# Kernel tuning notes

Hardware: AMD Instinct MI355X
Metric: run time of the kernel (lower is better)

Reference implementation:

```python
import jax, jax.numpy as jnp
import numpy as np

B, S, H, KV, D = 1, 2048, 32, 8, 128
HID = H * D
SINK, WIN, POOL = 128, 1024, 100
TAU = 1.0


def setup_inputs() -> dict:
    key = jax.random.key(0)
    ks = jax.random.split(key, 12)
    init = lambda k, shape: jax.random.normal(k, shape, jnp.float32) * 0.02
    return dict(
        hidden_states=jax.random.normal(ks[0], (B, S, HID), jnp.float32),
        Wq=init(ks[1], (HID, HID)),
        Wk=init(ks[2], (HID, KV * D)),
        Wv=init(ks[3], (HID, KV * D)),
        Wo=init(ks[4], (HID, HID)),
        fe1_w=init(ks[5], (D, 8 * D)), fe1_b=jnp.zeros((8 * D,), jnp.float32),
        fe2_w=init(ks[6], (8 * D, 2 * D)), fe2_b=jnp.zeros((2 * D,), jnp.float32),
        r1_w=init(ks[7], (2 * D, 4 * D)), r1_b=jnp.zeros((4 * D,), jnp.float32),
        r2_w=init(ks[8], (4 * D, D)), r2_b=jnp.zeros((D,), jnp.float32),
        r3_w=init(ks[9], (D, 1)), r3_b=jnp.zeros((1,), jnp.float32),
        router_noise=jax.random.uniform(ks[10], (B, 1), jnp.float32),
    )


def _rope(x):
    # x: [B,S,h,D]; non-interleaved (rotate-half) RoPE, base 10000
    half = D // 2
    inv_freq = 1.0 / (10000.0 ** (jnp.arange(0, D, 2, dtype=jnp.float32) / D))
    t = jnp.arange(S, dtype=jnp.float32)
    freqs = jnp.outer(t, inv_freq)  # [S, half]
    cos = jnp.cos(freqs)[None, :, None, :]
    sin = jnp.sin(freqs)[None, :, None, :]
    x1, x2 = x[..., :half], x[..., half:]
    return jnp.concatenate([x1 * cos - x2 * sin, x2 * cos + x1 * sin], axis=-1)


def reference(hidden_states, Wq, Wk, Wv, Wo, fe1_w, fe1_b, fe2_w, fe2_b,
              r1_w, r1_b, r2_w, r2_b, r3_w, r3_b, router_noise):
    q = (hidden_states @ Wq).reshape(B, S, H, D)
    k = (hidden_states @ Wk).reshape(B, S, KV, D)
    v = (hidden_states @ Wv).reshape(B, S, KV, D)
    q = _rope(q)
    k = _rope(k)
    # GQA: repeat kv heads
    kr = jnp.repeat(k, H // KV, axis=2)
    vr = jnp.repeat(v, H // KV, axis=2)
    scale = 1.0 / jnp.sqrt(jnp.float32(D))
    scores = jnp.einsum('bshd,bthd->bhst', q, kr) * scale  # [B,H,S,S]
    i = jnp.arange(S)[:, None]
    j = jnp.arange(S)[None, :]
    causal = j <= i
    # sink tokens + sliding window (streaming-LLM pattern)
    stream = causal & ((j < SINK) | (j > i - WIN))
    neg = jnp.float32(-1e30)
    p_full = jax.nn.softmax(jnp.where(causal, scores, neg), axis=-1)
    p_strm = jax.nn.softmax(jnp.where(stream, scores, neg), axis=-1)
    o_full = jnp.einsum('bhst,bthd->bshd', p_full, vr)
    o_strm = jnp.einsum('bhst,bthd->bshd', p_strm, vr)
    # Router: ctx_q pooling over first/last POOL query positions -> [B,H,D] -> [B,D]
    pooled = jnp.concatenate([q[:, :POOL], q[:, -POOL:]], axis=1).mean(axis=1)
    feat = pooled.mean(axis=1)  # [B,D]
    h1 = jax.nn.silu(feat @ fe1_w + fe1_b)
    h2 = h1 @ fe2_w + fe2_b
    h3 = jax.nn.silu(h2 @ r1_w + r1_b)
    h4 = jax.nn.silu(h3 @ r2_w + r2_b)
    logits = h4 @ r3_w + r3_b  # [B,1]
    eps = 1e-8
    g = -jnp.log(-jnp.log(router_noise + eps) + eps)
    z_soft = jax.nn.sigmoid((logits + g) / TAU)
    z_hard = (z_soft > 0.5).astype(z_soft.dtype)
    z = z_hard + z_soft - jax.lax.stop_gradient(z_soft)  # straight-through
    mix = z.reshape(B, 1, 1, 1)
    o = mix * o_strm + (1.0 - mix) * o_full  # gate sparse vs full retrieval
    return o.reshape(B, S, HID) @ Wo
```

## Files before the change

kernel.cpp:

```cpp
#include <hip/hip_runtime.h>
#include <hip/hip_bf16.h>

typedef unsigned short u16;
typedef unsigned int u32;
typedef __bf16 bf16x8 __attribute__((ext_vector_type(8)));
typedef float f32x4 __attribute__((ext_vector_type(4)));
typedef unsigned short u16x8 __attribute__((ext_vector_type(8)));

#define S_ 2048
#define H_ 32
#define KV_ 8
#define D_ 128
#define HID_ 4096
#define KVD_ 1024
#define QKVN 6144
#define SINK_ 128
#define WIN_ 1024
#define POOL_ 100
#define KVB 64

__device__ __forceinline__ u16 f2bf(float f) {
  union { float f; u32 u; } v; v.f = f;
  u32 r = v.u + 0x7FFFu + ((v.u >> 16) & 1u);
  return (u16)(r >> 16);
}
__device__ __forceinline__ float bf2f(u16 h) {
  union { u32 u; float f; } v; v.u = ((u32)h) << 16;
  return v.f;
}
__device__ __forceinline__ void glds16(const void* g, void* l) {
  __builtin_amdgcn_global_load_lds((__attribute__((address_space(1))) void*)g,
                                   (__attribute__((address_space(3))) void*)l, 16, 0, 0);
}

__device__ __forceinline__ void tr64(const float* __restrict__ W, u16* __restrict__ Wt,
                                     int K, int N, int nt, int kt, int tid, u16 T[64][66]) {
  const int r = tid >> 4, c4 = tid & 15;
#pragma unroll
  for (int p = 0; p < 4; ++p) {
    int row = p * 16 + r;
    float4 v = *(const float4*)&W[(size_t)(kt * 64 + row) * N + nt * 64 + c4 * 4];
    T[row][c4 * 4 + 0] = f2bf(v.x);
    T[row][c4 * 4 + 1] = f2bf(v.y);
    T[row][c4 * 4 + 2] = f2bf(v.z);
    T[row][c4 * 4 + 3] = f2bf(v.w);
  }
  __syncthreads();
  const int n = tid >> 3, c8 = tid & 7;
#pragma unroll
  for (int p = 0; p < 2; ++p) {
    int row = p * 32 + n;
    u16x8 o;
#pragma unroll
    for (int i = 0; i < 8; ++i) o[i] = T[c8 * 8 + i][row];
    *(u16x8*)&Wt[(size_t)(nt * 64 + row) * K + kt * 64 + c8 * 8] = o;
  }
}

__global__ __launch_bounds__(256) void k_prep(const float* __restrict__ hs, u16* __restrict__ hsb,
                                              const float* __restrict__ Wq, const float* __restrict__ Wk,
                                              const float* __restrict__ Wv, const float* __restrict__ Wo,
                                              u16* __restrict__ wqkv, u16* __restrict__ wot,
                                              float* __restrict__ cosT, float* __restrict__ sinT) {
  __shared__ u16 T[64][66];
  const int b = blockIdx.x, tid = threadIdx.x;
  if (b < 8192) {
    int i = b * 256 + tid;
    float4 v = ((const float4*)hs)[i];
    union { u16 s[4]; unsigned long long ll; } o;
    o.s[0] = f2bf(v.x); o.s[1] = f2bf(v.y); o.s[2] = f2bf(v.z); o.s[3] = f2bf(v.w);
    ((unsigned long long*)hsb)[i] = o.ll;
  } else if (b < 12288) {
    int id = b - 8192;
    tr64(Wq, wqkv, HID_, HID_, id % 64, id / 64, tid, T);
  } else if (b < 13312) {
    int id = b - 12288;
    tr64(Wk, wqkv + (size_t)4096 * HID_, HID_, KVD_, id % 16, id / 16, tid, T);
  } else if (b < 14336) {
    int id = b - 13312;
    tr64(Wv, wqkv + (size_t)5120 * HID_, HID_, KVD_, id % 16, id / 16, tid, T);
  } else if (b < 18432) {
    int id = b - 14336;
    tr64(Wo, wot, HID_, HID_, id % 64, id / 64, tid, T);
  } else {
    int idx = (b - 18432) * 256 + tid;
    int s = idx >> 6, i = idx & 63;
    float inv = powf(10000.f, -(float)i * (1.f / 64.f));
    float ang = (float)s * inv;
    cosT[idx] = cosf(ang);
    sinT[idx] = sinf(ang);
  }
}

__global__ void k_rope_q(u16* __restrict__ q, const float* __restrict__ cosT, const float* __restrict__ sinT) {
  int idx = blockIdx.x * 256 + threadIdx.x;
  if (idx >= S_ * H_ * 64) return;
  int i = idx & 63, h = (idx >> 6) & 31, s = idx >> 11;
  size_t base = (size_t)s * QKVN + h * D_ + i;
  float x1 = bf2f(q[base]), x2 = bf2f(q[base + 64]);
  float cs = cosT[(s << 6) + i], sn = sinT[(s << 6) + i];
  q[base] = f2bf(x1 * cs - x2 * sn);
  q[base + 64] = f2bf(x2 * cs + x1 * sn);
}

__global__ void k_rope_k(const u16* __restrict__ k, u16* __restrict__ kro,
                         const float* __restrict__ cosT, const float* __restrict__ sinT) {
  int idx = blockIdx.x * 256 + threadIdx.x;
  if (idx >= S_ * KV_ * 64) return;
  int i = idx & 63, kv = (idx >> 6) & 7, s = idx >> 9;
  float x1 = bf2f(k[(size_t)s * QKVN + 4096 + kv * D_ + i]);
  float x2 = bf2f(k[(size_t)s * QKVN + 4096 + kv * D_ + i + 64]);
  float cs = cosT[(s << 6) + i], sn = sinT[(s << 6) + i];
  size_t ob = (size_t)kv * S_ * D_ + (size_t)s * D_ + i;
  kro[ob] = f2bf(x1 * cs - x2 * sn);
  kro[ob + 64] = f2bf(x2 * cs + x1 * sn);
}

__global__ void k_transpose_v(const u16* __restrict__ v, u16* __restrict__ vt) {
  __shared__ u16 T[32][33];
  int st = blockIdx.x, dt = blockIdx.y, kv = blockIdx.z;
  int c = threadIdx.x & 31, r0 = threadIdx.x >> 5;
#pragma unroll
  for (int p = 0; p < 4; ++p) {
    int r = r0 + p * 8;
    T[r][c] = v[(size_t)(st * 32 + r) * QKVN + 5120 + kv * D_ + dt * 32 + c];
  }
  __syncthreads();
#pragma unroll
  for (int p = 0; p < 4; ++p) {
    int r = r0 + p * 8;
    vt[(size_t)kv * D_ * S_ + (size_t)(dt * 32 + r) * S_ + st * 32 + c] = T[c][r];
  }
}

__global__ void k_feat(const u16* __restrict__ q, float* __restrict__ feat) {
  int d = blockIdx.x, tid = threadIdx.x;
  float p = 0.f;
  for (int idx = tid; idx < 2 * POOL_ * H_; idx += 256) {
    int pos = idx >> 5, hh = idx & 31;
    int s = pos < POOL_ ? pos : (S_ - 2 * POOL_) + pos;
    p += bf2f(q[(size_t)s * QKVN + hh * D_ + d]);
  }
#pragma unroll
  for (int m = 1; m < 64; m <<= 1) p += __shfl_xor(p, m);
  __shared__ float red[4];
  if ((tid & 63) == 0) red[tid >> 6] = p;
  __syncthreads();
  if (tid == 0) feat[d] = (red[0] + red[1] + red[2] + red[3]) * (1.f / (2 * POOL_ * H_));
}

__global__ __launch_bounds__(256) void k_r1(const float* __restrict__ feat, const float* __restrict__ w,
                                            const float* __restrict__ b, float* __restrict__ h1) {
  __shared__ float fs[128];
  int tid = threadIdx.x;
  if (tid < 128) fs[tid] = feat[tid];
  __syncthreads();
  int o = blockIdx.x * 256 + tid;
  float a = b[o];
#pragma unroll 16
  for (int kk = 0; kk < 128; ++kk) a += fs[kk] * w[kk * 1024 + o];
  h1[o] = a / (1.f + expf(-a));
}
__global__ __launch_bounds__(256) void k_r2(const float* __restrict__ h1, const float* __restrict__ w,
                                            float* __restrict__ h2p) {
  __shared__ float hs[64];
  int tid = threadIdx.x, b = blockIdx.x;
  if (tid < 64) hs[tid] = h1[b * 64 + tid];
  __syncthreads();
  const float* wb = w + (size_t)b * 64 * 256 + tid;
  float p = 0.f;
#pragma unroll 16
  for (int kk = 0; kk < 64; ++kk) p += hs[kk] * wb[(size_t)kk * 256];
  h2p[b * 256 + tid] = p;
}
__global__ __launch_bounds__(256) void k_r3(const float* __restrict__ h2p, const float* __restrict__ b2,
                                            const float* __restrict__ w, const float* __restrict__ b3,
                                            float* __restrict__ h3) {
  __shared__ float h2s[256];
  int tid = threadIdx.x;
  float s = b2[tid];
#pragma unroll
  for (int j = 0; j < 16; ++j) s += h2p[j * 256 + tid];
  h2s[tid] = s;
  __syncthreads();
  int o = blockIdx.x * 256 + tid;
  float a = b3[o];
#pragma unroll 16
  for (int kk = 0; kk < 256; ++kk) a += h2s[kk] * w[kk * 512 + o];
  h3[o] = a / (1.f + expf(-a));
}
__global__ __launch_bounds__(256) void k_r45(const float* __restrict__ h3, const float* __restrict__ w4,
                                             const float* __restrict__ b4, const float* __restrict__ w5,
                                             const float* __restrict__ b5, const float* __restrict__ noise,
                                             float* __restrict__ mix) {
  __shared__ float h3s[512];
  __shared__ float hp[256];
  int tid = threadIdx.x;
  h3s[tid] = h3[tid];
  h3s[tid + 256] = h3[tid + 256];
  __syncthreads();
  int t = tid & 127, half = tid >> 7;
  float a = half ? 0.f : b4[t];
  const float* wcol = w4 + (size_t)(half << 8) * 128 + t;
  const float* hbase = h3s + (half << 8);
#pragma unroll 16
  for (int i = 0; i < 256; ++i) a += hbase[i] * wcol[(size_t)i * 128];
  hp[tid] = a;
  __syncthreads();
  if (tid < 128) {
    float v = hp[tid] + hp[tid + 128];
    float h4 = v / (1.f + expf(-v));
    hp[tid] = h4 * w5[tid];
  }
  __syncthreads();
  if (tid < 64) {
    float s = hp[tid] + hp[tid + 64];
#pragma unroll
    for (int m = 32; m >= 1; m >>= 1) s += __shfl_down(s, m);
    if (tid == 0) {
      float logits = s + b5[0];
      float u = noise[0];
      float g = -logf(-logf(u + 1e-8f) + 1e-8f);
      float zs = 1.f / (1.f + expf(-(logits + g)));
      mix[0] = zs > 0.5f ? 1.f : 0.f;
    }
  }
}

template <int MFRAG, int NFRAG>
__device__ __forceinline__ void stage_u(const u16* __restrict__ A, const u16* __restrict__ Bt,
                                        u16* buf, int m0, int n0, int K, int kg, int unit, int tid) {
  constexpr int AU = MFRAG / 2;
  constexpr int BM = MFRAG * 32;
  if (unit < AU) {
    int cell = unit * 512 + tid;
    int row = cell >> 3, c = cell & 7;
    glds16(A + (size_t)(m0 + row) * K + kg + ((c ^ (row & 7)) * 8),
           buf + ((size_t)(unit * 512 + (tid & ~63))) * 8);
  } else {
    int cell = (unit - AU) * 512 + tid;
    int row = cell >> 3, c = cell & 7;
    glds16(Bt + (size_t)(n0 + row) * K + kg + ((c ^ (row & 7)) * 8),
           buf + (size_t)BM * 64 + ((size_t)((unit - AU) * 512 + (tid & ~63))) * 8);
  }
}

template <int MFRAG, int NFRAG, int OUTF32>
__global__ __launch_bounds__(512, 1) void gemm_dp(const u16* __restrict__ A, const u16* __restrict__ Bt,
                                                  void* __restrict__ C, int M, int N, int K, int NTN) {
  constexpr int BM = MFRAG * 32;
  constexpr int BN = NFRAG * 64;
  constexpr int NH = NFRAG / 2;
  constexpr int U = MFRAG / 2 + NFRAG;
  static_assert(U == 8 || U == 6, "stage schedule assumes 6 or 8 units");
  constexpr int TE = (BM + BN) * 64;
  __shared__ __align__(16) u16 lds[2 * TE];
  const int tid = threadIdx.x, w = tid >> 6, ln = tid & 63;
  const int lr = ln & 15, lk = ln >> 4;
  const int wr = w >> 2, wc = w & 3;
  const int nwg = gridDim.x, cpx = nwg >> 3;
  const int wg = (blockIdx.x & 7) * cpx + (blockIdx.x >> 3);
  const int m0 = (wg / NTN) * BM, n0 = (wg % NTN) * BN;
  f32x4 acc[MFRAG][NFRAG];
#pragma unroll
  for (int i = 0; i < MFRAG; ++i)
#pragma unroll
    for (int j = 0; j < NFRAG; ++j) acc[i][j] = (f32x4){0.f, 0.f, 0.f, 0.f};
  const int nt = K / 64;

  auto ldA = [&](const u16* buf, bf16x8* af, int kh) {
#pragma unroll
    for (int mf = 0; mf < MFRAG; ++mf) {
      int row = wr * (MFRAG * 16) + mf * 16 + lr;
      af[mf] = *(const bf16x8*)&buf[row * 64 + (((kh * 4 + lk) ^ (row & 7)) * 8)];
    }
  };
  auto ldB = [&](const u16* buf, bf16x8* bp, int kh, int nh) {
#pragma unroll
    for (int nf = 0; nf < NH; ++nf) {
      int brow = wc * (NFRAG * 16) + (nh * NH + nf) * 16 + lr;
      bp[nf] = *(const bf16x8*)&buf[BM * 64 + brow * 64 + (((kh * 4 + lk) ^ (brow & 7)) * 8)];
    }
  };
  auto MMA = [&](const bf16x8* af, const bf16x8* bp, int nh) {
    __builtin_amdgcn_s_setprio(1);
#pragma unroll
    for (int mf = 0; mf < MFRAG; ++mf)
#pragma unroll
      for (int nf = 0; nf < NH; ++nf)
        acc[mf][nh * NH + nf] =
            __builtin_amdgcn_mfma_f32_16x16x32_bf16(af[mf], bp[nf], acc[mf][nh * NH + nf], 0, 0, 0);
    __builtin_amdgcn_s_setprio(0);
  };

#pragma unroll
  for (int i = 0; i < U; ++i) stage_u<MFRAG, NFRAG>(A, Bt, lds, m0, n0, K, 0, i, tid);
  stage_u<MFRAG, NFRAG>(A, Bt, lds + TE, m0, n0, K, 64, 0, tid);
  stage_u<MFRAG, NFRAG>(A, Bt, lds + TE, m0, n0, K, 64, 1, tid);
  asm volatile("s_waitcnt vmcnt(2)" ::: "memory");
  asm volatile("s_barrier" ::: "memory");
  bf16x8 afA[MFRAG], afB[MFRAG], b0[NH], b1[NH];
  ldA(lds, afA, 0);
  ldB(lds, b0, 0, 0);

  for (int t = 0; t < nt; ++t) {
    const u16* cb = lds + (t & 1) * TE;
    u16* nb = lds + ((t + 1) & 1) * TE;
    const bool hn = (t + 1 < nt);
    const int kn = (t + 1) * 64;
    asm volatile("s_barrier" ::: "memory");
    MMA(afA, b0, 0);
    ldB(cb, b1, 0, 1);
    if (hn) {
      stage_u<MFRAG, NFRAG>(A, Bt, nb, m0, n0, K, kn, 2, tid);
      stage_u<MFRAG, NFRAG>(A, Bt, nb, m0, n0, K, kn, 3, tid);
    }
    asm volatile("s_barrier" ::: "memory");
    MMA(afA, b1, 1);
    ldA(cb, afB, 1);
    ldB(cb, b0, 1, 0);
    if (hn) {
      stage_u<MFRAG, NFRAG>(A, Bt, nb, m0, n0, K, kn, 4, tid);
      stage_u<MFRAG, NFRAG>(A, Bt, nb, m0, n0, K, kn, 5, tid);
    }
    asm volatile("s_barrier" ::: "memory");
    MMA(afB, b0, 0);
    ldB(cb, b1, 1, 1);
    if (hn && U == 8) {
      stage_u<MFRAG, NFRAG>(A, Bt, nb, m0, n0, K, kn, 6, tid);
      stage_u<MFRAG, NFRAG>(A, Bt, nb, m0, n0, K, kn, 7, tid);
    }
    asm volatile("s_barrier" ::: "memory");
    MMA(afB, b1, 1);
    asm volatile("s_barrier" ::: "memory");
    if (hn) {
      if (t + 2 < nt) {
        stage_u<MFRAG, NFRAG>(A, Bt, (u16*)cb, m0, n0, K, (t + 2) * 64, 0, tid);
        stage_u<MFRAG, NFRAG>(A, Bt, (u16*)cb, m0, n0, K, (t + 2) * 64, 1, tid);
        asm volatile("s_waitcnt vmcnt(2)" ::: "memory");
      } else {
        asm volatile("s_waitcnt vmcnt(0)" ::: "memory");
      }
      asm volatile("s_barrier" ::: "memory");
      ldA(nb, afA, 0);
      ldB(nb, b0, 0, 0);
    }
  }
#pragma unroll
  for (int mf = 0; mf < MFRAG; ++mf) {
    int row = m0 + wr * (MFRAG * 16) + mf * 16 + lk * 4;
#pragma unroll
    for (int nf = 0; nf < NFRAG; ++nf) {
      int col = n0 + wc * (NFRAG * 16) + nf * 16 + lr;
#pragma unroll
      for (int jj = 0; jj < 4; ++jj) {
        float v = acc[mf][nf][jj];
        if (OUTF32) ((float*)C)[(size_t)(row + jj) * N + col] = v;
        else ((u16*)C)[(size_t)(row + jj) * N + col] = f2bf(v);
      }
    }
  }
}

__global__ __launch_bounds__(256) void k_attn(const u16* __restrict__ q, const u16* __restrict__ kr,
                                              const u16* __restrict__ vt, u16* __restrict__ o,
                                              const float* __restrict__ mixp, int qs) {
  __shared__ __align__(16) u16 Ks[2][KVB * 128];
  __shared__ __align__(16) u16 Vs[2][128 * KVB];
  __shared__ __align__(16) u16 Ps[4][16 * KVB];
  const int tid = threadIdx.x, w = tid >> 6, ln = tid & 63;
  const int lr = ln & 15, lk = ln >> 4;
  const int bid = blockIdx.x;
  const int qblk = (S_ / 64 - 1) - (bid >> 5);
  const int h = bid & 31, kv = h >> 2;
  const bool strm = (*mixp) > 0.5f;
  const int q0 = qblk * 64;
  const int qrow = q0 + w * 16 + lr;
  bf16x8 qf[4];
#pragma unroll
  for (int c = 0; c < 4; ++c)
    qf[c] = *(const bf16x8*)(q + (size_t)qrow * qs + h * D_ + c * 32 + lk * 8);
  f32x4 oacc[8];
#pragma unroll
  for (int c = 0; c < 8; ++c) oacc[c] = (f32x4){0.f, 0.f, 0.f, 0.f};
  float mrun[4], lrun[4];
#pragma unroll
  for (int j = 0; j < 4; ++j) { mrun[j] = -1e30f; lrun[j] = 0.f; }
  const u16* kbase = kr + (size_t)kv * S_ * D_;
  const u16* vbase = vt + (size_t)kv * D_ * S_;
  const int qg0 = q0 + w * 16 + lk * 4;
  const float scale = 0.08838834764831845f;

  auto stage = [&](int kt, int b) {
    const int kb0 = kt * KVB;
#pragma unroll
    for (int c = 0; c < 4; ++c) {
      int r0 = c * 16 + w * 4;
      int rg = r0 + (ln >> 4);
      int cg = (ln & 15) ^ (rg & 7);
      glds16(kbase + (size_t)(kb0 + rg) * D_ + cg * 8, &Ks[b][r0 * 128]);
    }
#pragma unroll
    for (int c = 0; c < 4; ++c) {
      int r0 = c * 32 + w * 8;
      int rg = r0 + (ln >> 3);
      int cg = (ln & 7) ^ (rg & 7);
      glds16(vbase + (size_t)rg * S_ + kb0 + cg * 8, &Vs[b][r0 * KVB]);
    }
  };
  auto nxt = [&](int k) {
    ++k;
    if (strm)
      while (k <= qblk && k * KVB >= SINK_ && k * KVB + KVB - 1 + WIN_ <= q0) ++k;
    return k;
  };

  int kt = 0, buf = 0;
  stage(0, 0);
  int ktn = nxt(0);
  while (kt <= qblk) {
    const bool hn = (ktn <= qblk);
    if (hn) {
      stage(ktn, buf ^ 1);
      asm volatile("s_waitcnt vmcnt(8)" ::: "memory");
    } else {
      asm volatile("s_waitcnt vmcnt(0)" ::: "memory");
    }
    asm volatile("s_barrier" ::: "memory");
    const int kb0 = kt * KVB;
    const u16* ks = Ks[buf];
    const u16* vs = Vs[buf];
    f32x4 sg[4];
#pragma unroll
    for (int g = 0; g < 4; ++g) sg[g] = (f32x4){0.f, 0.f, 0.f, 0.f};
    __builtin_amdgcn_s_setprio(1);
#pragma unroll
    for (int g = 0; g < 4; ++g) {
      int krow = g * 16 + lr;
      int sw = krow & 7;
#pragma unroll
      for (int c = 0; c < 4; ++c) {
        bf16x8 kf = *(const bf16x8*)&ks[krow * 128 + (((c * 4 + lk) ^ sw) * 8)];
        sg[g] = __builtin_amdgcn_mfma_f32_16x16x32_bf16(qf[c], kf, sg[g], 0, 0, 0);
      }
    }
    __builtin_amdgcn_s_setprio(0);
    const bool lastt = (kt == qblk);
    const bool needm = lastt ||
        (strm && !(kb0 + KVB <= SINK_ || kb0 >= q0 + 64 - WIN_));
    if (needm) {
#pragma unroll
      for (int g = 0; g < 4; ++g) {
        int kg = kb0 + g * 16 + lr;
#pragma unroll
        for (int j = 0; j < 4; ++j) {
          int qi = qg0 + j;
          float v = sg[g][j] * scale;
          bool ok = (kg <= qi) && (!strm || kg < SINK_ || kg > qi - WIN_);
          sg[g][j] = ok ? v : -1e30f;
        }
      }
    } else {
#pragma unroll
      for (int g = 0; g < 4; ++g)
#pragma unroll
        for (int j = 0; j < 4; ++j) sg[g][j] *= scale;
    }
    float rmax[4];
#pragma unroll
    for (int j = 0; j < 4; ++j)
      rmax[j] = fmaxf(fmaxf(sg[0][j], sg[1][j]), fmaxf(sg[2][j], sg[3][j]));
#pragma unroll
    for (int m2 = 1; m2 < 16; m2 <<= 1)
#pragma unroll
      for (int j = 0; j < 4; ++j) rmax[j] = fmaxf(rmax[j], __shfl_xor(rmax[j], m2));
    float dmax = rmax[0] - mrun[0];
#pragma unroll
    for (int j = 1; j < 4; ++j) dmax = fmaxf(dmax, rmax[j] - mrun[j]);
    if (!__all(dmax <= 8.f)) {
      float corr[4];
#pragma unroll
      for (int j = 0; j < 4; ++j) {
        float mn = fmaxf(mrun[j], rmax[j]);
        corr[j] = __expf(mrun[j] - mn);
        mrun[j] = mn;
        lrun[j] *= corr[j];
      }
#pragma unroll
      for (int c = 0; c < 8; ++c) {
        f32x4 t2 = oacc[c];
        t2[0] *= corr[0]; t2[1] *= corr[1]; t2[2] *= corr[2]; t2[3] *= corr[3];
        oacc[c] = t2;
      }
    }
    float rsum[4] = {0.f, 0.f, 0.f, 0.f};
#pragma unroll
    for (int g = 0; g < 4; ++g)
#pragma unroll
      for (int j = 0; j < 4; ++j) {
        float p = __expf(sg[g][j] - mrun[j]);
        sg[g][j] = p;
        rsum[j] += p;
      }
#pragma unroll
    for (int m2 = 1; m2 < 16; m2 <<= 1)
#pragma unroll
      for (int j = 0; j < 4; ++j) rsum[j] += __shfl_xor(rsum[j], m2);
#pragma unroll
    for (int j = 0; j < 4; ++j) lrun[j] += rsum[j];
#pragma unroll
    for (int g = 0; g < 4; ++g) {
      int col = g * 16 + lr;
      int c16 = col >> 3;
#pragma unroll
      for (int j = 0; j < 4; ++j) {
        int row = lk * 4 + j;
        Ps[w][row * KVB + ((c16 ^ (row & 7)) * 8) + (col & 7)] = f2bf(sg[g][j]);
      }
    }
    __builtin_amdgcn_s_setprio(1);
#pragma unroll
    for (int half = 0; half < 2; ++half) {
      bf16x8 pf = *(const bf16x8*)&Ps[w][lr * KVB + (((half * 4 + lk) ^ (lr & 7)) * 8)];
#pragma unroll
      for (int cc = 0; cc < 8; ++cc) {
        int vrow = cc * 16 + lr;
        bf16x8 vf = *(const bf16x8*)&vs[vrow * KVB + (((half * 4 + lk) ^ (vrow & 7)) * 8)];
        oacc[cc] = __builtin_amdgcn_mfma_f32_16x16x32_bf16(pf, vf, oacc[cc], 0, 0, 0);
      }
    }
    __builtin_amdgcn_s_setprio(0);
    asm volatile("s_barrier" ::: "memory");
    kt = ktn;
    ktn = nxt(ktn);
    buf ^= 1;
  }
#pragma unroll
  for (int cc = 0; cc < 8; ++cc)
#pragma unroll
    for (int j = 0; j < 4; ++j) {
      float ov = oacc[cc][j] / lrun[j];
      o[(size_t)(qg0 + j) * HID_ + h * D_ + cc * 16 + lr] = f2bf(ov);
    }
}

extern "C" void kernel_launch(void* const* d_in, const int* in_sizes, int n_in,
                              void* d_out, int out_size, void* d_ws, size_t ws_size,
                              hipStream_t stream) {
  const float* hs = (const float*)d_in[0];
  const float* Wq = (const float*)d_in[1];
  const float* Wk = (const float*)d_in[2];
  const float* Wv = (const float*)d_in[3];
  const float* Wo = (const float*)d_in[4];
  const float* fe1_w = (const float*)d_in[5];
  const float* fe1_b = (const float*)d_in[6];
  const float* fe2_w = (const float*)d_in[7];
  const float* fe2_b = (const float*)d_in[8];
  const float* r1_w = (const float*)d_in[9];
  const float* r1_b = (const float*)d_in[10];
  const float* r2_w = (const float*)d_in[11];
  const float* r2_b = (const float*)d_in[12];
  const float* r3_w = (const float*)d_in[13];
  const float* r3_b = (const float*)d_in[14];
  const float* noise = (const float*)d_in[15];

  char* ws = (char*)d_ws;
  size_t off = 0;
  auto alloc = [&](size_t b) { char* p = ws + off; off += (b + 255) & ~(size_t)255; return p; };
  u16* hsb = (u16*)alloc((size_t)S_ * HID_ * 2);
  u16* wqkv = (u16*)alloc((size_t)QKVN * HID_ * 2);
  u16* qkvbuf = (u16*)alloc((size_t)S_ * QKVN * 2);
  u16* wot = (u16*)alloc((size_t)HID_ * HID_ * 2);
  u16* krbuf = (u16*)alloc((size_t)S_ * KVD_ * 2);
  u16* vtbuf = (u16*)alloc((size_t)S_ * KVD_ * 2);
  u16* obuf = (u16*)alloc((size_t)S_ * HID_ * 2);
  float* cosT = (float*)alloc((size_t)S_ * 64 * 4);
  float* sinT = (float*)alloc((size_t)S_ * 64 * 4);
  float* feat = (float*)alloc(512);
  float* mix = (float*)alloc(256);
  float* h1buf = (float*)alloc(1024 * 4);
  float* h2p = (float*)alloc(16 * 256 * 4);
  float* h3buf = (float*)alloc(512 * 4);

  k_prep<<<dim3(18944), dim3(256), 0, stream>>>(hs, hsb, Wq, Wk, Wv, Wo, wqkv, wot, cosT, sinT);

  gemm_dp<4, 6, 0><<<dim3(256), dim3(512), 0, stream>>>(hsb, wqkv, (void*)qkvbuf,
                                                        S_, QKVN, HID_, QKVN / 384);

  k_rope_q<<<dim3(S_ * H_ * 64 / 256), dim3(256), 0, stream>>>(qkvbuf, cosT, sinT);
  k_rope_k<<<dim3(S_ * KV_ * 64 / 256), dim3(256), 0, stream>>>(qkvbuf, krbuf, cosT, sinT);
  k_transpose_v<<<dim3(S_ / 32, D_ / 32, KV_), dim3(256), 0, stream>>>(qkvbuf, vtbuf);

  k_feat<<<dim3(D_), dim3(256), 0, stream>>>(qkvbuf, feat);
  k_r1<<<dim3(4), dim3(256), 0, stream>>>(feat, fe1_w, fe1_b, h1buf);
  k_r2<<<dim3(16), dim3(256), 0, stream>>>(h1buf, fe2_w, h2p);
  k_r3<<<dim3(2), dim3(256), 0, stream>>>(h2p, fe2_b, r1_w, r1_b, h3buf);
  k_r45<<<dim3(1), dim3(256), 0, stream>>>(h3buf, r2_w, r2_b, r3_w, r3_b, noise, mix);

  k_attn<<<dim3((S_ / 64) * H_), dim3(256), 0, stream>>>(qkvbuf, krbuf, vtbuf, obuf, mix, QKVN);

  gemm_dp<4, 4, 1><<<dim3(256), dim3(512), 0, stream>>>(obuf, wot, d_out,
                                                        S_, HID_, HID_, HID_ / 256);
}
```

Before: 368.9 us.

## Fuse RoPE/transpose kernels and restructure GEMM main loop to two MMA phases

Merges the Q RoPE, K RoPE and V transpose launches into one kernel that splits work by block index, removing two kernel launches. Separately, the GEMM inner loop moves from four MMA phases (half of the N fragments per phase) to two phases over all N fragments. This cuts barriers per k-tile and reorders when the global-to-LDS stage loads are issued. The trade-off is more live B-fragment registers and a coarser interleaving of loads with MFMA work.

```diff
diff --git a/kernel.cpp b/kernel.cpp
--- a/kernel.cpp
+++ b/kernel.cpp
@@ -92,44 +92,43 @@
   }
 }
 
-__global__ void k_rope_q(u16* __restrict__ q, const float* __restrict__ cosT, const float* __restrict__ sinT) {
-  int idx = blockIdx.x * 256 + threadIdx.x;
-  if (idx >= S_ * H_ * 64) return;
-  int i = idx & 63, h = (idx >> 6) & 31, s = idx >> 11;
-  size_t base = (size_t)s * QKVN + h * D_ + i;
-  float x1 = bf2f(q[base]), x2 = bf2f(q[base + 64]);
-  float cs = cosT[(s << 6) + i], sn = sinT[(s << 6) + i];
-  q[base] = f2bf(x1 * cs - x2 * sn);
-  q[base + 64] = f2bf(x2 * cs + x1 * sn);
-}
-
-__global__ void k_rope_k(const u16* __restrict__ k, u16* __restrict__ kro,
-                         const float* __restrict__ cosT, const float* __restrict__ sinT) {
-  int idx = blockIdx.x * 256 + threadIdx.x;
-  if (idx >= S_ * KV_ * 64) return;
-  int i = idx & 63, kv = (idx >> 6) & 7, s = idx >> 9;
-  float x1 = bf2f(k[(size_t)s * QKVN + 4096 + kv * D_ + i]);
-  float x2 = bf2f(k[(size_t)s * QKVN + 4096 + kv * D_ + i + 64]);
-  float cs = cosT[(s << 6) + i], sn = sinT[(s << 6) + i];
-  size_t ob = (size_t)kv * S_ * D_ + (size_t)s * D_ + i;
-  kro[ob] = f2bf(x1 * cs - x2 * sn);
-  kro[ob + 64] = f2bf(x2 * cs + x1 * sn);
-}
-
-__global__ void k_transpose_v(const u16* __restrict__ v, u16* __restrict__ vt) {
+__global__ __launch_bounds__(256) void k_pos(u16* __restrict__ qkv, u16* __restrict__ kro,
+                                             u16* __restrict__ vt,
+                                             const float* __restrict__ cosT, const float* __restrict__ sinT) {
   __shared__ u16 T[32][33];
-  int st = blockIdx.x, dt = blockIdx.y, kv = blockIdx.z;
-  int c = threadIdx.x & 31, r0 = threadIdx.x >> 5;
-#pragma unroll
-  for (int p = 0; p < 4; ++p) {
-    int r = r0 + p * 8;
-    T[r][c] = v[(size_t)(st * 32 + r) * QKVN + 5120 + kv * D_ + dt * 32 + c];
-  }
-  __syncthreads();
-#pragma unroll
-  for (int p = 0; p < 4; ++p) {
-    int r = r0 + p * 8;
-    vt[(size_t)kv * D_ * S_ + (size_t)(dt * 32 + r) * S_ + st * 32 + c] = T[c][r];
+  const int b = blockIdx.x, tid = threadIdx.x;
+  if (b < 16384) {
+    int idx = b * 256 + tid;
+    int i = idx & 63, h = (idx >> 6) & 31, s = idx >> 11;
+    size_t base = (size_t)s * QKVN + h * D_ + i;
+    float x1 = bf2f(qkv[base]), x2 = bf2f(qkv[base + 64]);
+    float cs = cosT[(s << 6) + i], sn = sinT[(s << 6) + i];
+    qkv[base] = f2bf(x1 * cs - x2 * sn);
+    qkv[base + 64] = f2bf(x2 * cs + x1 * sn);
+  } else if (b < 20480) {
+    int idx = (b - 16384) * 256 + tid;
+    int i = idx & 63, kv = (idx >> 6) & 7, s = idx >> 9;
+    float x1 = bf2f(qkv[(size_t)s * QKVN + 4096 + kv * D_ + i]);
+    float x2 = bf2f(qkv[(size_t)s * QKVN + 4096 + kv * D_ + i + 64]);
+    float cs = cosT[(s << 6) + i], sn = sinT[(s << 6) + i];
+    size_t ob = (size_t)kv * S_ * D_ + (size_t)s * D_ + i;
+    kro[ob] = f2bf(x1 * cs - x2 * sn);
+    kro[ob + 64] = f2bf(x2 * cs + x1 * sn);
+  } else {
+    int id = b - 20480;
+    int st = id & 63, dt = (id >> 6) & 3, kv = id >> 8;
+    int c = tid & 31, r0 = tid >> 5;
+#pragma unroll
+    for (int p = 0; p < 4; ++p) {
+      int r = r0 + p * 8;
+      T[r][c] = qkv[(size_t)(st * 32 + r) * QKVN + 5120 + kv * D_ + dt * 32 + c];
+    }
+    __syncthreads();
+#pragma unroll
+    for (int p = 0; p < 4; ++p) {
+      int r = r0 + p * 8;
+      vt[(size_t)kv * D_ * S_ + (size_t)(dt * 32 + r) * S_ + st * 32 + c] = T[c][r];
+    }
   }
 }
 
@@ -250,7 +249,6 @@
                                                   void* __restrict__ C, int M, int N, int K, int NTN) {
   constexpr int BM = MFRAG * 32;
   constexpr int BN = NFRAG * 64;
-  constexpr int NH = NFRAG / 2;
   constexpr int U = MFRAG / 2 + NFRAG;
   static_assert(U == 8 || U == 6, "stage schedule assumes 6 or 8 units");
   constexpr int TE = (BM + BN) * 64;
@@ -275,21 +273,20 @@
       af[mf] = *(const bf16x8*)&buf[row * 64 + (((kh * 4 + lk) ^ (row & 7)) * 8)];
     }
   };
-  auto ldB = [&](const u16* buf, bf16x8* bp, int kh, int nh) {
-#pragma unroll
-    for (int nf = 0; nf < NH; ++nf) {
-      int brow = wc * (NFRAG * 16) + (nh * NH + nf) * 16 + lr;
+  auto ldB = [&](const u16* buf, bf16x8* bp, int kh) {
+#pragma unroll
+    for (int nf = 0; nf < NFRAG; ++nf) {
+      int brow = wc * (NFRAG * 16) + nf * 16 + lr;
       bp[nf] = *(const bf16x8*)&buf[BM * 64 + brow * 64 + (((kh * 4 + lk) ^ (brow & 7)) * 8)];
     }
   };
-  auto MMA = [&](const bf16x8* af, const bf16x8* bp, int nh) {
+  auto MMA = [&](const bf16x8* af, const bf16x8* bp) {
     __builtin_amdgcn_s_setprio(1);
 #pragma unroll
     for (int mf = 0; mf < MFRAG; ++mf)
 #pragma unroll
-      for (int nf = 0; nf < NH; ++nf)
-        acc[mf][nh * NH + nf] =
-            __builtin_amdgcn_mfma_f32_16x16x32_bf16(af[mf], bp[nf], acc[mf][nh * NH + nf], 0, 0, 0);
+      for (int nf = 0; nf < NFRAG; ++nf)
+        acc[mf][nf] = __builtin_amdgcn_mfma_f32_16x16x32_bf16(af[mf], bp[nf], acc[mf][nf], 0, 0, 0);
     __builtin_amdgcn_s_setprio(0);
   };
 
@@ -299,9 +296,9 @@
   stage_u<MFRAG, NFRAG>(A, Bt, lds + TE, m0, n0, K, 64, 1, tid);
   asm volatile("s_waitcnt vmcnt(2)" ::: "memory");
   asm volatile("s_barrier" ::: "memory");
-  bf16x8 afA[MFRAG], afB[MFRAG], b0[NH], b1[NH];
+  bf16x8 afA[MFRAG], afB[MFRAG], bA[NFRAG], bB[NFRAG];
   ldA(lds, afA, 0);
-  ldB(lds, b0, 0, 0);
+  ldB(lds, bA, 0);
 
   for (int t = 0; t < nt; ++t) {
     const u16* cb = lds + (t & 1) * TE;
@@ -309,29 +306,20 @@
     const bool hn = (t + 1 < nt);
     const int kn = (t + 1) * 64;
     asm volatile("s_barrier" ::: "memory");
-    MMA(afA, b0, 0);
-    ldB(cb, b1, 0, 1);
+    MMA(afA, bA);
+    ldA(cb, afB, 1);
+    ldB(cb, bB, 1);
     if (hn) {
       stage_u<MFRAG, NFRAG>(A, Bt, nb, m0, n0, K, kn, 2, tid);
       stage_u<MFRAG, NFRAG>(A, Bt, nb, m0, n0, K, kn, 3, tid);
+      stage_u<MFRAG, NFRAG>(A, Bt, nb, m0, n0, K, kn, 4, tid);
     }
     asm volatile("s_barrier" ::: "memory");
-    MMA(afA, b1, 1);
-    ldA(cb, afB, 1);
-    ldB(cb, b0, 1, 0);
+    MMA(afB, bB);
     if (hn) {
-      stage_u<MFRAG, NFRAG>(A, Bt, nb, m0, n0, K, kn, 4, tid);
-      stage_u<MFRAG, NFRAG>(A, Bt, nb, m0, n0, K, kn, 5, tid);
-    }
-    asm volatile("s_barrier" ::: "memory");
-    MMA(afB, b0, 0);
-    ldB(cb, b1, 1, 1);
-    if (hn && U == 8) {
-      stage_u<MFRAG, NFRAG>(A, Bt, nb, m0, n0, K, kn, 6, tid);
-      stage_u<MFRAG, NFRAG>(A, Bt, nb, m0, n0, K, kn, 7, tid);
-    }
-    asm volatile("s_barrier" ::: "memory");
-    MMA(afB, b1, 1);
+#pragma unroll
+      for (int i = 5; i < U; ++i) stage_u<MFRAG, NFRAG>(A, Bt, nb, m0, n0, K, kn, i, tid);
+    }
     asm volatile("s_barrier" ::: "memory");
     if (hn) {
       if (t + 2 < nt) {
@@ -343,7 +331,7 @@
       }
       asm volatile("s_barrier" ::: "memory");
       ldA(nb, afA, 0);
-      ldB(nb, b0, 0, 0);
+      ldB(nb, bA, 0);
     }
   }
 #pragma unroll
@@ -587,9 +575,7 @@
   gemm_dp<4, 6, 0><<<dim3(256), dim3(512), 0, stream>>>(hsb, wqkv, (void*)qkvbuf,
                                                         S_, QKVN, HID_, QKVN / 384);
 
-  k_rope_q<<<dim3(S_ * H_ * 64 / 256), dim3(256), 0, stream>>>(qkvbuf, cosT, sinT);
-  k_rope_k<<<dim3(S_ * KV_ * 64 / 256), dim3(256), 0, stream>>>(qkvbuf, krbuf, cosT, sinT);
-  k_transpose_v<<<dim3(S_ / 32, D_ / 32, KV_), dim3(256), 0, stream>>>(qkvbuf, vtbuf);
+  k_pos<<<dim3(22528), dim3(256), 0, stream>>>(qkvbuf, krbuf, vtbuf, cosT, sinT);
 
   k_feat<<<dim3(D_), dim3(256), 0, stream>>>(qkvbuf, feat);
   k_r1<<<dim3(4), dim3(256), 0, stream>>>(feat, fe1_w, fe1_b, h1buf);
```

Measured after the change: 382.9 us. 3.8% more time.
